# Kernel tuning notes

Measured on AMD Instinct MI355X. Metric: run time of the kernel, lower is better.

Reference implementation:

```python
import jax, jax.numpy as jnp
import numpy as np


def hard_sigmoid(x):
    # Keras hard_sigmoid: clip(0.2*x + 0.5, 0, 1)
    return jnp.clip(x * 0.2 + 0.5, 0.0, 1.0)


def conv2d_same(x, w):
    # x: [B,H,W,Cin], w: [kh,kw,Cin,Cout]
    return jax.lax.conv_general_dilated(
        x, w, window_strides=(1, 1), padding='SAME',
        dimension_numbers=('NHWC', 'HWIO', 'NHWC'))


def convlstm2d(x, Wx, Wh, b):
    # x: [B,T,H,W,Cin]; Wx: [k,k,Cin,4*Cout]; Wh: [k,k,Cout,4*Cout]; b: [4*Cout]
    B, T, H, W, _ = x.shape
    Cout = Wh.shape[2]
    h0 = jnp.zeros((B, H, W, Cout), x.dtype)
    c0 = jnp.zeros((B, H, W, Cout), x.dtype)

    def step(carry, xt):
        h, c = carry
        z = conv2d_same(xt, Wx) + conv2d_same(h, Wh) + b
        i, f, g, o = jnp.split(z, 4, axis=-1)  # Keras gate order i,f,c,o
        c = hard_sigmoid(f) * c + hard_sigmoid(i) * jnp.tanh(g)
        h = hard_sigmoid(o) * jnp.tanh(c)
        return (h, c), h

    _, hs = jax.lax.scan(step, (h0, c0), jnp.moveaxis(x, 1, 0))
    return jnp.moveaxis(hs, 0, 1)  # [B,T,H,W,Cout]


def bn_inference(x, gamma, beta, mean, var, eps=1e-3):
    # Keras BatchNormalization default eps=1e-3, inference mode (training=False)
    return (x - mean) * jax.lax.rsqrt(var + eps) * gamma + beta


def upsample_2x2(x):
    # UpSampling3D(size=(1,2,2)) on [B,T,H,W,C]
    return jnp.repeat(jnp.repeat(x, 2, axis=2), 2, axis=3)


def deconv_block(x, Wx, Wh, b, g, be, mm, mv):
    return upsample_2x2(bn_inference(convlstm2d(x, Wx, Wh, b), g, be, mm, mv))


def setup_inputs() -> dict:
    key = jax.random.key(0)
    ks = jax.random.split(key, 32)
    B, T, H, W = 2, 8, 16, 16
    Cin = 192
    chans = [128, 64, 32]
    K = 3
    d = {'x': jax.random.normal(ks[0], (B, T, H, W, Cin), jnp.float32)}
    ci = Cin
    ki = 1
    for l, co in enumerate(chans, start=1):
        d[f'Wx{l}'] = jax.random.normal(ks[ki], (K, K, ci, 4 * co), jnp.float32) * 0.05; ki += 1
        d[f'Wh{l}'] = jax.random.normal(ks[ki], (K, K, co, 4 * co), jnp.float32) * 0.05; ki += 1
        d[f'b{l}'] = jnp.zeros((4 * co,), jnp.float32)
        d[f'g{l}'] = jax.random.uniform(ks[ki], (co,), jnp.float32) + 0.5; ki += 1
        d[f'be{l}'] = jax.random.normal(ks[ki], (co,), jnp.float32) * 0.1; ki += 1
        d[f'mm{l}'] = jax.random.normal(ks[ki], (co,), jnp.float32) * 0.1; ki += 1
        d[f'mv{l}'] = jax.random.uniform(ks[ki], (co,), jnp.float32) + 0.5; ki += 1
        ci = co
    return d


def reference(x, Wx1, Wh1, b1, g1, be1, mm1, mv1,
              Wx2, Wh2, b2, g2, be2, mm2, mv2,
              Wx3, Wh3, b3, g3, be3, mm3, mv3):
    x = deconv_block(x, Wx1, Wh1, b1, g1, be1, mm1, mv1)  # [2,8,32,32,128]
    x = deconv_block(x, Wx2, Wh2, b2, g2, be2, mm2, mv2)  # [2,8,64,64,64]
    x = deconv_block(x, Wx3, Wh3, b3, g3, be3, mm3, mv3)  # [2,8,128,128,32]
    return x
```

## Files before the change

kernel.cpp:

```cpp
#include <hip/hip_runtime.h>
#include <math.h>

#define BATCH 2
#define TSTEPS 8

typedef __attribute__((ext_vector_type(8))) short s16x8;
typedef __attribute__((ext_vector_type(4))) float f32x4;

__device__ __forceinline__ float hsig(float v){ return fminf(fmaxf(0.2f*v+0.5f,0.f),1.f); }
__device__ __forceinline__ ushort f2bf(float f){
    uint u = __builtin_bit_cast(uint, f);
    u = (u + 0x7FFFu + ((u >> 16) & 1u)) >> 16;
    return (ushort)u;
}
__device__ __forceinline__ uint pack2bf(float lo, float hi){
    return (uint)f2bf(lo) | ((uint)f2bf(hi) << 16);
}

template<int KCH, int Co>
__device__ __forceinline__ void packw(const float* __restrict__ W, ushort* __restrict__ dst, int d){
    int j = d & 7, lane = (d >> 3) & 63;
    int q = lane >> 4, l = lane & 15;
    int rest = d >> 9;
    int c = rest % KCH, t_n = rest / KCH;
    int k = c*32 + q*8 + j;
    int np = t_n*16 + l;
    int g = np & 3, co = np >> 2;
    dst[d] = f2bf(W[(size_t)k*(4*Co) + g*Co + co]);
}

#define SZ_X    786432
#define SZ_WX1  884736
#define SZ_WH1  589824
#define SZ_WX2  294912
#define SZ_WH2  147456
#define SZ_WX3  73728
#define SZ_WH3  36864
#define SZ_PREP (SZ_X+SZ_WX1+SZ_WH1+SZ_WX2+SZ_WH2+SZ_WX3+SZ_WH3)

__global__ void prep_kernel(const float* __restrict__ x,
    const float* __restrict__ Wx1, const float* __restrict__ Wh1,
    const float* __restrict__ Wx2, const float* __restrict__ Wh2,
    const float* __restrict__ Wx3, const float* __restrict__ Wh3,
    ushort* __restrict__ xpad,
    ushort* __restrict__ Wxp1, ushort* __restrict__ Whp1,
    ushort* __restrict__ Wxp2, ushort* __restrict__ Whp2,
    ushort* __restrict__ Wxp3, ushort* __restrict__ Whp3)
{
    int i = blockIdx.x * 256 + threadIdx.x;
    if (i < SZ_X){
        int c = i % 192; int r = i / 192;
        int xx = r % 16; r /= 16; int yy = r % 16; int bt = r / 16;
        xpad[((size_t)bt*18*18 + (yy+1)*18 + (xx+1))*192 + c] = f2bf(x[i]);
        return;
    } i -= SZ_X;
    if (i < SZ_WX1){ packw<54,128>(Wx1, Wxp1, i); return; } i -= SZ_WX1;
    if (i < SZ_WH1){ packw<36,128>(Wh1, Whp1, i); return; } i -= SZ_WH1;
    if (i < SZ_WX2){ packw<36, 64>(Wx2, Wxp2, i); return; } i -= SZ_WX2;
    if (i < SZ_WH2){ packw<18, 64>(Wh2, Whp2, i); return; } i -= SZ_WH2;
    if (i < SZ_WX3){ packw<18, 32>(Wx3, Wxp3, i); return; } i -= SZ_WX3;
    if (i < SZ_WH3){ packw< 9, 32>(Wh3, Whp3, i); }
}

template<int CI, int CO, int H, int W>
__global__ __launch_bounds__(256) void convx_k(
    const ushort* __restrict__ Apad, const ushort* __restrict__ Wpk,
    const float* __restrict__ bias, float* __restrict__ Zx)
{
    constexpr int W_T = (W < 32) ? W : 32;
    constexpr int ROWS = 32 / W_T;
    constexpr int PR = ROWS + 2, PPX = W_T + 2;
    constexpr int PCI = CI + 8;
    constexpr int KCH = 9*CI/32, CPT = CI/32;
    constexpr int HW = H*W, HP = H+2, WP = W+2;
    constexpr int N4 = 4*CO;
    constexpr int CH8 = CI/8;
    constexpr int TOT = PR*PPX*CH8;

    __shared__ ushort patch[PR*PPX*PCI];
    __shared__ float Zsc[32][132];

    const int tid = threadIdx.x, lane = tid & 63, wave = tid >> 6;
    const int quad = lane >> 4, l16 = lane & 15;
    const int m0 = blockIdx.x * 32;
    const int bt = m0 / HW, rem = m0 - bt*HW;
    const int y0 = rem / W, x0 = rem - (rem/W)*W;

    const ushort* gsrc = Apad + (size_t)bt*HP*WP*CI;
    for (int c = tid; c < TOT; c += 256){
        int pix = c / CH8, ch = c - pix*CH8;
        int prow = pix / PPX, ppx = pix - prow*PPX;
        *(uint4*)&patch[pix*PCI + ch*8] =
            *(const uint4*)(gsrc + ((size_t)(y0+prow)*WP + (x0+ppx))*CI + ch*8);
    }
    __syncthreads();

    const int tn0 = blockIdx.y*8 + wave*2;
    const ushort* bptr0 = Wpk + ((size_t)tn0*KCH*64 + lane)*8;
    const ushort* bptr1 = Wpk + ((size_t)(tn0+1)*KCH*64 + lane)*8;

    int labase[2];
    #pragma unroll
    for (int s = 0; s < 2; ++s){
        int p = s*16 + l16;
        int rp = p / W_T, xp = p - rp*W_T;
        labase[s] = (rp*PPX + xp)*PCI + quad*8;
    }

    f32x4 acc[2][2] = {};
    #pragma unroll
    for (int it = 0; it < KCH; ++it){
        const int tap = it / CPT, ci0 = (it - tap*CPT)*32;
        const int kh = tap/3, kw = tap - (tap/3)*3;
        const int off = (kh*PPX + kw)*PCI + ci0;
        s16x8 b0 = *(const s16x8*)(bptr0 + (size_t)it*512);
        s16x8 b1 = *(const s16x8*)(bptr1 + (size_t)it*512);
        s16x8 a0 = *(const s16x8*)&patch[labase[0] + off];
        s16x8 a1 = *(const s16x8*)&patch[labase[1] + off];
        acc[0][0] = __builtin_amdgcn_mfma_f32_16x16x32_bf16(a0, b0, acc[0][0], 0,0,0);
        acc[0][1] = __builtin_amdgcn_mfma_f32_16x16x32_bf16(a0, b1, acc[0][1], 0,0,0);
        acc[1][0] = __builtin_amdgcn_mfma_f32_16x16x32_bf16(a1, b0, acc[1][0], 0,0,0);
        acc[1][1] = __builtin_amdgcn_mfma_f32_16x16x32_bf16(a1, b1, acc[1][1], 0,0,0);
    }

    #pragma unroll
    for (int s = 0; s < 2; ++s){
        #pragma unroll
        for (int nt = 0; nt < 2; ++nt){
            const int col = blockIdx.y*128 + wave*32 + nt*16 + l16;
            const float bv = bias[(col & 3)*CO + (col >> 2)];
            #pragma unroll
            for (int r = 0; r < 4; ++r)
                Zsc[s*16 + quad*4 + r][wave*32 + nt*16 + l16] = acc[s][nt][r] + bv;
        }
    }
    __syncthreads();

    #pragma unroll
    for (int i = 0; i < 4; ++i){
        int c = i*256 + tid;
        int row = c >> 5, cc = (c & 31) << 2;
        *(float4*)&Zx[(size_t)(m0+row)*N4 + blockIdx.y*128 + cc] = *(float4*)&Zsc[row][cc];
    }
}

template<int CI, int CO, int H, int W>
__device__ __forceinline__ void conv_slice_role(char* smem, int lbid, int t,
    const ushort* __restrict__ Apad, const ushort* __restrict__ Wpk,
    const float* __restrict__ bias, float* __restrict__ Zx)
{
    constexpr int W_T = (W < 32) ? W : 32;
    constexpr int PR = (32/W_T) + 2, PPX = W_T + 2;
    constexpr int PCI = CI + 8;
    constexpr int KCH = 9*CI/32, CPT = CI/32;
    constexpr int HW = H*W, HP = H+2, WP = W+2;
    constexpr int N4 = 4*CO;
    constexpr int CH8 = CI/8;
    constexpr int TOT = PR*PPX*CH8;
    constexpr int TPB = HW/32;
    constexpr int PXT = 2*TPB;

    ushort* patch = (ushort*)smem;
    float* Zsc = (float*)(smem + PR*PPX*PCI*2);

    const int tid = threadIdx.x, lane = tid & 63, wave = tid >> 6;
    const int quad = lane >> 4, l16 = lane & 15;
    const int lx = lbid % PXT, ly = lbid / PXT;
    const int b = lx / TPB;
    const int idx0 = (lx - b*TPB)*32;
    const int bt = b*TSTEPS + t;
    const int m0 = bt*HW + idx0;
    const int y0 = idx0 / W, x0 = idx0 - (idx0/W)*W;

    const ushort* gsrc = Apad + (size_t)bt*HP*WP*CI;
    for (int c = tid; c < TOT; c += 256){
        int pix = c / CH8, ch = c - pix*CH8;
        int prow = pix / PPX, ppx = pix - prow*PPX;
        *(uint4*)&patch[pix*PCI + ch*8] =
            *(const uint4*)(gsrc + ((size_t)(y0+prow)*WP + (x0+ppx))*CI + ch*8);
    }
    __syncthreads();

    const int tn0 = ly*8 + wave*2;
    const ushort* bptr0 = Wpk + ((size_t)tn0*KCH*64 + lane)*8;
    const ushort* bptr1 = Wpk + ((size_t)(tn0+1)*KCH*64 + lane)*8;

    int labase[2];
    #pragma unroll
    for (int s = 0; s < 2; ++s){
        int p = s*16 + l16;
        int rp = p / W_T, xp = p - rp*W_T;
        labase[s] = (rp*PPX + xp)*PCI + quad*8;
    }

    f32x4 acc[2][2] = {};
    #pragma unroll
    for (int it = 0; it < KCH; ++it){
        const int tap = it / CPT, ci0 = (it - tap*CPT)*32;
        const int kh = tap/3, kw = tap - (tap/3)*3;
        const int off = (kh*PPX + kw)*PCI + ci0;
        s16x8 b0 = *(const s16x8*)(bptr0 + (size_t)it*512);
        s16x8 b1 = *(const s16x8*)(bptr1 + (size_t)it*512);
        s16x8 a0 = *(const s16x8*)&patch[labase[0] + off];
        s16x8 a1 = *(const s16x8*)&patch[labase[1] + off];
        acc[0][0] = __builtin_amdgcn_mfma_f32_16x16x32_bf16(a0, b0, acc[0][0], 0,0,0);
        acc[0][1] = __builtin_amdgcn_mfma_f32_16x16x32_bf16(a0, b1, acc[0][1], 0,0,0);
        acc[1][0] = __builtin_amdgcn_mfma_f32_16x16x32_bf16(a1, b0, acc[1][0], 0,0,0);
        acc[1][1] = __builtin_amdgcn_mfma_f32_16x16x32_bf16(a1, b1, acc[1][1], 0,0,0);
    }

    #pragma unroll
    for (int s = 0; s < 2; ++s){
        #pragma unroll
        for (int nt = 0; nt < 2; ++nt){
            const int col = ly*128 + wave*32 + nt*16 + l16;
            const float bv = bias[(col & 3)*CO + (col >> 2)];
            #pragma unroll
            for (int r = 0; r < 4; ++r)
                Zsc[(s*16 + quad*4 + r)*132 + wave*32 + nt*16 + l16] = acc[s][nt][r] + bv;
        }
    }
    __syncthreads();

    #pragma unroll
    for (int i = 0; i < 4; ++i){
        int c = i*256 + tid;
        int row = c >> 5, cc = (c & 31) << 2;
        *(float4*)&Zx[(size_t)(m0+row)*N4 + ly*128 + cc] = *(float4*)&Zsc[row*132 + cc];
    }
}

template<int CO, int H, int W, int OUT_BF16>
__device__ __forceinline__ void step_role(char* smem, int lbid, int t, int first,
    const float* __restrict__ Zx, const ushort* __restrict__ Whpk,
    const ushort* __restrict__ hprev, ushort* __restrict__ hnew,
    float* __restrict__ cst,
    const float* __restrict__ gamma, const float* __restrict__ beta,
    const float* __restrict__ mmean, const float* __restrict__ mvar,
    void* __restrict__ outp)
{
    constexpr int W_T = (W < 32) ? W : 32;
    constexpr int PR = (32/W_T) + 2, PPX = W_T + 2;
    constexpr int PCO = CO + 8;
    constexpr int KCH = 9*CO/32, CPT = CO/32;
    constexpr int NJ = (KCH + 3)/4;
    constexpr int HW = H*W, HP = H+2, WP = W+2;
    constexpr int N4 = 4*CO;
    constexpr int CH8 = CO/8;
    constexpr int TOT = PR*PPX*CH8;
    constexpr int PT = (BATCH*HW)/32;

    ushort* patch = (ushort*)smem;
    float* Zs = (float*)(smem + PR*PPX*PCO*2);
    float* Hs = (float*)(smem + PR*PPX*PCO*2 + 18432);

    const int tid = threadIdx.x, lane = tid & 63, wave = tid >> 6;
    const int quad = lane >> 4, l16 = lane & 15;
    const int pxt = lbid % PT, colIdx = lbid / PT;
    const int m0 = pxt * 32;
    const int b2 = m0 / HW, rem = m0 - b2*HW;
    const int y0 = rem / W, x0 = rem - (rem/W)*W;
    const int co0 = colIdx * 8;

    if (!first){
        const ushort* gsrc = hprev + (size_t)b2*HP*WP*CO;
        for (int c = tid; c < TOT; c += 256){
            int pix = c / CH8, ch = c - pix*CH8;
            int prow = pix / PPX, ppx = pix - prow*PPX;
            *(uint4*)&patch[pix*PCO + ch*8] =
                *(const uint4*)(gsrc + ((size_t)(y0+prow)*WP + (x0+ppx))*CO + ch*8);
        }
        __syncthreads();

        const int tn0 = colIdx*2;
        const ushort* bptr0 = Whpk + ((size_t)tn0*KCH*64 + lane)*8;
        const ushort* bptr1 = Whpk + ((size_t)(tn0+1)*KCH*64 + lane)*8;

        int labase[2];
        #pragma unroll
        for (int s = 0; s < 2; ++s){
            int p = s*16 + l16;
            int rp = p / W_T, xp = p - rp*W_T;
            labase[s] = (rp*PPX + xp)*PCO + quad*8;
        }

        f32x4 acc[2][2] = {};
        const int nj = (KCH - wave + 3) >> 2;
        #pragma unroll
        for (int j = 0; j < NJ; ++j){
            if (j < nj){
                const int it = wave + 4*j;
                const int tap = it / CPT, ci0 = (it - tap*CPT)*32;
                const int kh = tap/3, kw = tap - (tap/3)*3;
                const int off = (kh*PPX + kw)*PCO + ci0;
                s16x8 b0 = *(const s16x8*)(bptr0 + (size_t)it*512);
                s16x8 b1 = *(const s16x8*)(bptr1 + (size_t)it*512);
                s16x8 a0 = *(const s16x8*)&patch[labase[0] + off];
                s16x8 a1 = *(const s16x8*)&patch[labase[1] + off];
                acc[0][0] = __builtin_amdgcn_mfma_f32_16x16x32_bf16(a0, b0, acc[0][0], 0,0,0);
                acc[0][1] = __builtin_amdgcn_mfma_f32_16x16x32_bf16(a0, b1, acc[0][1], 0,0,0);
                acc[1][0] = __builtin_amdgcn_mfma_f32_16x16x32_bf16(a1, b0, acc[1][0], 0,0,0);
                acc[1][1] = __builtin_amdgcn_mfma_f32_16x16x32_bf16(a1, b1, acc[1][1], 0,0,0);
            }
        }
        #pragma unroll
        for (int s = 0; s < 2; ++s)
            #pragma unroll
            for (int nt = 0; nt < 2; ++nt)
                #pragma unroll
                for (int r = 0; r < 4; ++r)
                    Zs[(wave*32 + s*16 + quad*4 + r)*36 + nt*16 + l16] = acc[s][nt][r];
        __syncthreads();
    }

    {
        const int px = tid >> 3, coin = tid & 7;
        const int m = m0 + px;
        const int rr = m - b2*HW;
        const int co = co0 + coin;
        const size_t zrow = (size_t)(b2*TSTEPS + t)*HW + rr;
        const float4 zx = *(const float4*)&Zx[zrow*N4 + colIdx*32 + coin*4];
        float zi = zx.x, zf = zx.y, zg = zx.z, zo = zx.w;
        if (!first){
            #pragma unroll
            for (int w = 0; w < 4; ++w){
                const float4 s = *(const float4*)&Zs[(w*32 + px)*36 + coin*4];
                zi += s.x; zf += s.y; zg += s.z; zo += s.w;
            }
        }
        const float iv = hsig(zi), fv = hsig(zf);
        const float gv = tanhf(zg), ov = hsig(zo);
        const float cold = first ? 0.f : cst[(size_t)m*CO + co];
        const float cn = fv*cold + iv*gv;
        cst[(size_t)m*CO + co] = cn;
        const float h = ov * tanhf(cn);
        const int y = rr / W, x = rr - (rr/W)*W;
        hnew[((size_t)b2*HP*WP + (y+1)*WP + (x+1))*CO + co] = f2bf(h);
        Hs[px*8 + coin] = (h - mmean[co])*rsqrtf(mvar[co]+1e-3f)*gamma[co] + beta[co];
    }
    __syncthreads();

    if (OUT_BF16){
        if (tid < 128){
            const int px = tid >> 2, q = tid & 3;
            const int ypos = q >> 1, xpos = q & 1;
            const int m = m0 + px;
            const int rr = m - b2*HW;
            const int y = rr / W, x = rr - (rr/W)*W;
            const float* hs = &Hs[px*8];
            uint4 v;
            v.x = pack2bf(hs[0], hs[1]); v.y = pack2bf(hs[2], hs[3]);
            v.z = pack2bf(hs[4], hs[5]); v.w = pack2bf(hs[6], hs[7]);
            ushort* o = (ushort*)outp;
            const size_t opix = ((size_t)(b2*TSTEPS + t)*(2*H+2) + 2*y+1+ypos)*(size_t)(2*W+2) + 2*x+1+xpos;
            *(uint4*)&o[opix*CO + co0] = v;
        }
    } else {
        const int px = tid >> 3, q = (tid >> 1) & 3, half = tid & 1;
        const int ypos = q >> 1, xpos = q & 1;
        const int m = m0 + px;
        const int rr = m - b2*HW;
        const int y = rr / W, x = rr - (rr/W)*W;
        float4 v = *(const float4*)&Hs[px*8 + half*4];
        float* o = (float*)outp;
        const size_t opix = ((size_t)(b2*TSTEPS + t)*(2*H) + 2*y+ypos)*(size_t)(2*W) + 2*x+xpos;
        *(float4*)&o[opix*CO + co0 + half*4] = v;
    }
}

__global__ __launch_bounds__(256) void mega(
    int e1, int e2, int e3, int e4,
    int t1, int t2, int t3, int t4, int t5,
    int f1, int f2, int f3,
    const float* Zx1, const ushort* Whp1, const ushort* h1p, ushort* h1n, float* c1,
    const float* g1, const float* be1, const float* mm1, const float* mv1, ushort* x2pad,
    const ushort* Wxp2, const float* b2v, float* Zx2,
    const ushort* Whp2, const ushort* h2p, ushort* h2n, float* c2,
    const float* g2, const float* be2, const float* mm2, const float* mv2, ushort* x3pad,
    const ushort* Wxp3, const float* b3v, float* Zx3,
    const ushort* Whp3, const ushort* h3p, ushort* h3n, float* c3,
    const float* g3, const float* be3, const float* mm3, const float* mv3, float* outp)
{
    __shared__ __align__(16) char smem[44672];
    const int bid = blockIdx.x;
    if (bid < e1){
        step_role<128,16,16,1>(smem, bid, t1, f1, Zx1, Whp1, h1p, h1n, c1, g1, be1, mm1, mv1, x2pad);
        return;
    }
    if (bid < e2){
        conv_slice_role<128,64,32,32>(smem, bid - e1, t2, x2pad, Wxp2, b2v, Zx2);
        return;
    }
    if (bid < e3){
        step_role<64,32,32,1>(smem, bid - e2, t3, f2, Zx2, Whp2, h2p, h2n, c2, g2, be2, mm2, mv2, x3pad);
        return;
    }
    if (bid < e4){
        conv_slice_role<64,32,64,64>(smem, bid - e3, t4, x3pad, Wxp3, b3v, Zx3);
        return;
    }
    step_role<32,64,64,0>(smem, bid - e4, t5, f3, Zx3, Whp3, h3p, h3n, c3, g3, be3, mm3, mv3, outp);
}

extern "C" void kernel_launch(void* const* d_in, const int* in_sizes, int n_in,
                              void* d_out, int out_size, void* d_ws, size_t ws_size,
                              hipStream_t stream) {
    const float* x   = (const float*)d_in[0];
    const float* Wx1 = (const float*)d_in[1];  const float* Wh1 = (const float*)d_in[2];
    const float* b1  = (const float*)d_in[3];  const float* g1  = (const float*)d_in[4];
    const float* be1 = (const float*)d_in[5];  const float* mm1 = (const float*)d_in[6];
    const float* mv1 = (const float*)d_in[7];
    const float* Wx2 = (const float*)d_in[8];  const float* Wh2 = (const float*)d_in[9];
    const float* b2  = (const float*)d_in[10]; const float* g2  = (const float*)d_in[11];
    const float* be2 = (const float*)d_in[12]; const float* mm2 = (const float*)d_in[13];
    const float* mv2 = (const float*)d_in[14];
    const float* Wx3 = (const float*)d_in[15]; const float* Wh3 = (const float*)d_in[16];
    const float* b3  = (const float*)d_in[17]; const float* g3  = (const float*)d_in[18];
    const float* be3 = (const float*)d_in[19]; const float* mm3 = (const float*)d_in[20];
    const float* mv3 = (const float*)d_in[21];

    char* ws = (char*)d_ws;
    size_t off = 0;
    auto alloc = [&](size_t bytes) { char* p = ws + off; off += (bytes + 255) & ~(size_t)255; return p; };

    float*  Zx1 = (float*)alloc(2097152ull * 4);
    float*  Zx2 = (float*)alloc(4194304ull * 4);
    float*  Zx3 = (float*)alloc(8388608ull * 4);
    float*  c1  = (float*)alloc(65536ull * 4);
    float*  c2  = (float*)alloc(131072ull * 4);
    float*  c3  = (float*)alloc(262144ull * 4);

    char* zbase = alloc(17685504ull);
    ushort* xpad  = (ushort*)zbase;
    ushort* x2pad = xpad  + 995328;
    ushort* x3pad = x2pad + 2367488;
    ushort* h1A   = x3pad + 4460544;
    ushort* h1B   = h1A + 82944;
    ushort* h2A   = h1B + 82944;
    ushort* h2B   = h2A + 147968;
    ushort* h3A   = h2B + 147968;
    ushort* h3B   = h3A + 278784;

    ushort* Wxp1 = (ushort*)alloc(884736ull * 2);
    ushort* Wxp2 = (ushort*)alloc(294912ull * 2);
    ushort* Wxp3 = (ushort*)alloc(73728ull * 2);
    ushort* Whp1 = (ushort*)alloc(589824ull * 2);
    ushort* Whp2 = (ushort*)alloc(147456ull * 2);
    ushort* Whp3 = (ushort*)alloc(36864ull * 2);

    hipMemsetAsync(zbase, 0, 17685504ull, stream);

    prep_kernel<<<(SZ_PREP + 255) / 256, 256, 0, stream>>>(
        x, Wx1, Wh1, Wx2, Wh2, Wx3, Wh3,
        xpad, Wxp1, Whp1, Wxp2, Whp2, Wxp3, Whp3);

    convx_k<192, 128, 16, 16><<<dim3(128, 4), 256, 0, stream>>>(xpad, Wxp1, b1, Zx1);

    for (int j = 0; j < 12; ++j){
        const int a1 = (j < 8),            t1 = a1 ? j     : 0;
        const int a2 = (j >= 1 && j <= 8), tc2 = a2 ? j - 1 : 0;
        const int a3 = (j >= 2 && j <= 9), ts2 = a3 ? j - 2 : 0;
        const int a4 = (j >= 3 && j <= 10), tc3 = a4 ? j - 3 : 0;
        const int a5 = (j >= 4),           ts3 = a5 ? j - 4 : 0;

        const int e1 = a1 ? 256 : 0;
        const int e2 = e1 + (a2 ? 128 : 0);
        const int e3 = e2 + (a3 ? 512 : 0);
        const int e4 = e3 + (a4 ? 256 : 0);
        const int e5 = e4 + (a5 ? 1024 : 0);
        if (e5 == 0) continue;

        const ushort* h1p = (t1 & 1) ? h1B : h1A;  ushort* h1n = (t1 & 1) ? h1A : h1B;
        const ushort* h2p = (ts2 & 1) ? h2B : h2A; ushort* h2n = (ts2 & 1) ? h2A : h2B;
        const ushort* h3p = (ts3 & 1) ? h3B : h3A; ushort* h3n = (ts3 & 1) ? h3A : h3B;

        mega<<<dim3(e5), 256, 0, stream>>>(
            e1, e2, e3, e4,
            t1, tc2, ts2, tc3, ts3,
            (t1 == 0), (ts2 == 0), (ts3 == 0),
            Zx1, Whp1, h1p, h1n, c1, g1, be1, mm1, mv1, x2pad,
            Wxp2, b2, Zx2,
            Whp2, h2p, h2n, c2, g2, be2, mm2, mv2, x3pad,
            Wxp3, b3, Zx3,
            Whp3, h3p, h3n, c3, g3, be3, mm3, mv3, (float*)d_out);
    }
}
```

Measured before the change: 277.5 us.

## Restructure LSTM step blocks to split N tiles across waves with register-level gate epilogue

```diff
diff --git a/kernel.cpp b/kernel.cpp
--- a/kernel.cpp
+++ b/kernel.cpp
@@ -230,8 +230,8 @@
     }
 }
 
-template<int CO, int H, int W, int OUT_BF16>
-__device__ __forceinline__ void step_role(char* smem, int lbid, int t, int first,
+template<int CO, int H, int W, int OUT_BF16, int NTW>
+__device__ __forceinline__ void step_role2(char* smem, int lbid, int t, int first,
     const float* __restrict__ Zx, const ushort* __restrict__ Whpk,
     const ushort* __restrict__ hprev, ushort* __restrict__ hnew,
     float* __restrict__ cst,
@@ -243,7 +243,6 @@
     constexpr int PR = (32/W_T) + 2, PPX = W_T + 2;
     constexpr int PCO = CO + 8;
     constexpr int KCH = 9*CO/32, CPT = CO/32;
-    constexpr int NJ = (KCH + 3)/4;
     constexpr int HW = H*W, HP = H+2, WP = W+2;
     constexpr int N4 = 4*CO;
     constexpr int CH8 = CO/8;
@@ -251,8 +250,6 @@
     constexpr int PT = (BATCH*HW)/32;
 
     ushort* patch = (ushort*)smem;
-    float* Zs = (float*)(smem + PR*PPX*PCO*2);
-    float* Hs = (float*)(smem + PR*PPX*PCO*2 + 18432);
 
     const int tid = threadIdx.x, lane = tid & 63, wave = tid >> 6;
     const int quad = lane >> 4, l16 = lane & 15;
@@ -260,7 +257,9 @@
     const int m0 = pxt * 32;
     const int b2 = m0 / HW, rem = m0 - b2*HW;
     const int y0 = rem / W, x0 = rem - (rem/W)*W;
-    const int co0 = colIdx * 8;
+    const int tile0 = colIdx*(4*NTW) + wave*NTW;
+
+    f32x4 acc[2][NTW] = {};
 
     if (!first){
         const ushort* gsrc = hprev + (size_t)b2*HP*WP*CO;
@@ -272,9 +271,10 @@
         }
         __syncthreads();
 
-        const int tn0 = colIdx*2;
-        const ushort* bptr0 = Whpk + ((size_t)tn0*KCH*64 + lane)*8;
-        const ushort* bptr1 = Whpk + ((size_t)(tn0+1)*KCH*64 + lane)*8;
+        const ushort* bptr[NTW];
+        #pragma unroll
+        for (int nt = 0; nt < NTW; ++nt)
+            bptr[nt] = Whpk + ((size_t)(tile0+nt)*KCH*64 + lane)*8;
 
         int labase[2];
         #pragma unroll
@@ -284,87 +284,68 @@
             labase[s] = (rp*PPX + xp)*PCO + quad*8;
         }
 
-        f32x4 acc[2][2] = {};
-        const int nj = (KCH - wave + 3) >> 2;
-        #pragma unroll
-        for (int j = 0; j < NJ; ++j){
-            if (j < nj){
-                const int it = wave + 4*j;
-                const int tap = it / CPT, ci0 = (it - tap*CPT)*32;
-                const int kh = tap/3, kw = tap - (tap/3)*3;
-                const int off = (kh*PPX + kw)*PCO + ci0;
-                s16x8 b0 = *(const s16x8*)(bptr0 + (size_t)it*512);
-                s16x8 b1 = *(const s16x8*)(bptr1 + (size_t)it*512);
-                s16x8 a0 = *(const s16x8*)&patch[labase[0] + off];
-                s16x8 a1 = *(const s16x8*)&patch[labase[1] + off];
-                acc[0][0] = __builtin_amdgcn_mfma_f32_16x16x32_bf16(a0, b0, acc[0][0], 0,0,0);
-                acc[0][1] = __builtin_amdgcn_mfma_f32_16x16x32_bf16(a0, b1, acc[0][1], 0,0,0);
-                acc[1][0] = __builtin_amdgcn_mfma_f32_16x16x32_bf16(a1, b0, acc[1][0], 0,0,0);
-                acc[1][1] = __builtin_amdgcn_mfma_f32_16x16x32_bf16(a1, b1, acc[1][1], 0,0,0);
+        #pragma unroll
+        for (int it = 0; it < KCH; ++it){
+            const int tap = it / CPT, ci0 = (it - tap*CPT)*32;
+            const int kh = tap/3, kw = tap - (tap/3)*3;
+            const int off = (kh*PPX + kw)*PCO + ci0;
+            s16x8 a0 = *(const s16x8*)&patch[labase[0] + off];
+            s16x8 a1 = *(const s16x8*)&patch[labase[1] + off];
+            #pragma unroll
+            for (int nt = 0; nt < NTW; ++nt){
+                s16x8 bb = *(const s16x8*)(bptr[nt] + (size_t)it*512);
+                acc[0][nt] = __builtin_amdgcn_mfma_f32_16x16x32_bf16(a0, bb, acc[0][nt], 0,0,0);
+                acc[1][nt] = __builtin_amdgcn_mfma_f32_16x16x32_bf16(a1, bb, acc[1][nt], 0,0,0);
             }
         }
-        #pragma unroll
-        for (int s = 0; s < 2; ++s)
+    }
+
+    const int g = l16 & 3;
+    const size_t zbase = (size_t)(b2*TSTEPS + t)*HW;
+
+    #pragma unroll
+    for (int nt = 0; nt < NTW; ++nt){
+        const int tile = tile0 + nt;
+        const int co = tile*4 + (l16 >> 2);
+        const int col4 = tile*16 + (l16 & 12);
+        const float sc = gamma[co]*rsqrtf(mvar[co]+1e-3f);
+        const float sh = beta[co] - mmean[co]*sc;
+        #pragma unroll
+        for (int s = 0; s < 2; ++s){
             #pragma unroll
-            for (int nt = 0; nt < 2; ++nt)
-                #pragma unroll
-                for (int r = 0; r < 4; ++r)
-                    Zs[(wave*32 + s*16 + quad*4 + r)*36 + nt*16 + l16] = acc[s][nt][r];
-        __syncthreads();
-    }
-
-    {
-        const int px = tid >> 3, coin = tid & 7;
-        const int m = m0 + px;
-        const int rr = m - b2*HW;
-        const int co = co0 + coin;
-        const size_t zrow = (size_t)(b2*TSTEPS + t)*HW + rr;
-        const float4 zx = *(const float4*)&Zx[zrow*N4 + colIdx*32 + coin*4];
-        float zi = zx.x, zf = zx.y, zg = zx.z, zo = zx.w;
-        if (!first){
-            #pragma unroll
-            for (int w = 0; w < 4; ++w){
-                const float4 s = *(const float4*)&Zs[(w*32 + px)*36 + coin*4];
-                zi += s.x; zf += s.y; zg += s.z; zo += s.w;
+            for (int r = 0; r < 4; ++r){
+                const int px = s*16 + quad*4 + r;
+                const int m = m0 + px;
+                const int rr = m - b2*HW;
+                const float4 zx = *(const float4*)&Zx[(zbase + rr)*N4 + col4];
+                const float zsel = (g==0) ? zx.x : (g==1) ? zx.y : (g==2) ? zx.z : zx.w;
+                const float z = zsel + acc[s][nt][r];
+                const float v = (g==2) ? tanhf(z) : hsig(z);
+                const float iv = __shfl_xor(v, g);
+                const float fv = __shfl_xor(v, g^1);
+                const float gv = __shfl_xor(v, g^2);
+                const float ov = __shfl_xor(v, g^3);
+                const float cold = first ? 0.f : cst[(size_t)m*CO + co];
+                const float cn = fv*cold + iv*gv;
+                const float h = ov * tanhf(cn);
+                const int y = rr / W, x = rr - (rr/W)*W;
+                if (g == 0){
+                    cst[(size_t)m*CO + co] = cn;
+                    hnew[((size_t)b2*HP*WP + (y+1)*WP + (x+1))*CO + co] = f2bf(h);
+                }
+                const float hb = h*sc + sh;
+                const int ypos = g >> 1, xpos = g & 1;
+                if (OUT_BF16){
+                    ushort* o = (ushort*)outp;
+                    const size_t opix = ((size_t)(b2*TSTEPS + t)*(2*H+2) + 2*y+1+ypos)*(size_t)(2*W+2) + 2*x+1+xpos;
+                    o[opix*CO + co] = f2bf(hb);
+                } else {
+                    float* o = (float*)outp;
+                    const size_t opix = ((size_t)(b2*TSTEPS + t)*(2*H) + 2*y+ypos)*(size_t)(2*W) + 2*x+xpos;
+                    o[opix*CO + co] = hb;
+                }
             }
         }
-        const float iv = hsig(zi), fv = hsig(zf);
-        const float gv = tanhf(zg), ov = hsig(zo);
-        const float cold = first ? 0.f : cst[(size_t)m*CO + co];
-        const float cn = fv*cold + iv*gv;
-        cst[(size_t)m*CO + co] = cn;
-        const float h = ov * tanhf(cn);
-        const int y = rr / W, x = rr - (rr/W)*W;
-        hnew[((size_t)b2*HP*WP + (y+1)*WP + (x+1))*CO + co] = f2bf(h);
-        Hs[px*8 + coin] = (h - mmean[co])*rsqrtf(mvar[co]+1e-3f)*gamma[co] + beta[co];
-    }
-    __syncthreads();
-
-    if (OUT_BF16){
-        if (tid < 128){
-            const int px = tid >> 2, q = tid & 3;
-            const int ypos = q >> 1, xpos = q & 1;
-            const int m = m0 + px;
-            const int rr = m - b2*HW;
-            const int y = rr / W, x = rr - (rr/W)*W;
-            const float* hs = &Hs[px*8];
-            uint4 v;
-            v.x = pack2bf(hs[0], hs[1]); v.y = pack2bf(hs[2], hs[3]);
-            v.z = pack2bf(hs[4], hs[5]); v.w = pack2bf(hs[6], hs[7]);
-            ushort* o = (ushort*)outp;
-            const size_t opix = ((size_t)(b2*TSTEPS + t)*(2*H+2) + 2*y+1+ypos)*(size_t)(2*W+2) + 2*x+1+xpos;
-            *(uint4*)&o[opix*CO + co0] = v;
-        }
-    } else {
-        const int px = tid >> 3, q = (tid >> 1) & 3, half = tid & 1;
-        const int ypos = q >> 1, xpos = q & 1;
-        const int m = m0 + px;
-        const int rr = m - b2*HW;
-        const int y = rr / W, x = rr - (rr/W)*W;
-        float4 v = *(const float4*)&Hs[px*8 + half*4];
-        float* o = (float*)outp;
-        const size_t opix = ((size_t)(b2*TSTEPS + t)*(2*H) + 2*y+ypos)*(size_t)(2*W) + 2*x+xpos;
-        *(float4*)&o[opix*CO + co0 + half*4] = v;
     }
 }
 
@@ -384,7 +365,7 @@
     __shared__ __align__(16) char smem[44672];
     const int bid = blockIdx.x;
     if (bid < e1){
-        step_role<128,16,16,1>(smem, bid, t1, f1, Zx1, Whp1, h1p, h1n, c1, g1, be1, mm1, mv1, x2pad);
+        step_role2<128,16,16,1,2>(smem, bid, t1, f1, Zx1, Whp1, h1p, h1n, c1, g1, be1, mm1, mv1, x2pad);
         return;
     }
     if (bid < e2){
@@ -392,14 +373,14 @@
         return;
     }
     if (bid < e3){
-        step_role<64,32,32,1>(smem, bid - e2, t3, f2, Zx2, Whp2, h2p, h2n, c2, g2, be2, mm2, mv2, x3pad);
+        step_role2<64,32,32,1,4>(smem, bid - e2, t3, f2, Zx2, Whp2, h2p, h2n, c2, g2, be2, mm2, mv2, x3pad);
         return;
     }
     if (bid < e4){
         conv_slice_role<64,32,64,64>(smem, bid - e3, t4, x3pad, Wxp3, b3v, Zx3);
         return;
     }
-    step_role<32,64,64,0>(smem, bid - e4, t5, f3, Zx3, Whp3, h3p, h3n, c3, g3, be3, mm3, mv3, outp);
+    step_role2<32,64,64,0,2>(smem, bid - e4, t5, f3, Zx3, Whp3, h3p, h3n, c3, g3, be3, mm3, mv3, outp);
 }
 
 extern "C" void kernel_launch(void* const* d_in, const int* in_sizes, int n_in,
@@ -463,11 +444,11 @@
         const int a4 = (j >= 3 && j <= 10), tc3 = a4 ? j - 3 : 0;
         const int a5 = (j >= 4),           ts3 = a5 ? j - 4 : 0;
 
-        const int e1 = a1 ? 256 : 0;
+        const int e1 = a1 ? 64 : 0;
         const int e2 = e1 + (a2 ? 128 : 0);
-        const int e3 = e2 + (a3 ? 512 : 0);
+        const int e3 = e2 + (a3 ? 64 : 0);
         const int e4 = e3 + (a4 ? 256 : 0);
-        const int e5 = e4 + (a5 ? 1024 : 0);
+        const int e5 = e4 + (a5 ? 256 : 0);
         if (e5 == 0) continue;
 
         const ushort* h1p = (t1 & 1) ? h1B : h1A;  ushort* h1n = (t1 & 1) ? h1A : h1B;
```

Result: slower. 490.9 us (+76.9%).
